# Performance work log

Measured on AMD Instinct MI355X. Metric: run time of the kernel, lower is better.

Reference implementation:

```python
import jax, jax.numpy as jnp
import numpy as np

EPS = 1e-6

def elu_feature_map(x):
    return jax.nn.elu(x) + 1.0

def setup_inputs() -> dict:
    key = jax.random.key(0)
    kq, kk, kv = jax.random.split(key, 3)
    N, L, S, H, D = 8, 8192, 8192, 8, 32
    return {
        "queries": jax.random.normal(kq, (N, L, H, D), dtype=jnp.float32),
        "keys": jax.random.normal(kk, (N, S, H, D), dtype=jnp.float32),
        "values": jax.random.normal(kv, (N, S, H, D), dtype=jnp.float32),
    }

def reference(queries, keys, values):
    # Linear (kernelized) attention, default path of MixAttention.forward
    Q = elu_feature_map(queries)            # [N,L,H,D]
    K = elu_feature_map(keys)               # [N,S,H,D]
    v_length = values.shape[1]
    vals = values / v_length                # [N,S,H,D]
    KV = jnp.einsum('nshd,nshv->nhdv', K, vals)          # [N,H,D,D]
    Z = 1.0 / (jnp.einsum('nlhd,nhd->nlh', Q, K.sum(axis=1)) + EPS)  # [N,L,H]
    out = jnp.einsum('nlhd,nhdv,nlh->nlhv', Q, KV, Z) * v_length     # [N,L,H,D]
    return out
```

## Files before the change

kernel.cpp:

```cpp
#include <hip/hip_runtime.h>


constexpr int N_ = 8, L_ = 8192, S_ = 8192, H_ = 8, D_ = 32;
constexpr int NH = N_ * H_;
constexpr int PART_STRIDE = D_ * D_ + D_;
constexpr int LCH = 256;
constexpr float EPS_ = 1e-6f;
constexpr int HD = H_ * D_;

__device__ __forceinline__ float fmap(float x) {
    return x > 0.0f ? x + 1.0f : __expf(x);
}

template<int SPLIT>
__global__ __launch_bounds__(512, 4) void lin_attn_phase1(
        const float* __restrict__ Kg, const float* __restrict__ Vg,
        float* __restrict__ part) {
    constexpr int CS = S_ / SPLIT;
    const int blk = blockIdx.x;
    const int n  = blk / SPLIT;
    const int sc = blk % SPLIT;
    const int t = threadIdx.x;
    const int w = t >> 6;
    const int j = t & 63;
    const int half = j >> 5;
    const int jj = j & 31;
    const int d0 = (jj & 7) << 2;
    const int v0 = (jj >> 3) << 3;

    float acc[4][8];
    #pragma unroll
    for (int a = 0; a < 4; ++a)
        #pragma unroll
        for (int b = 0; b < 8; ++b) acc[a][b] = 0.0f;
    float kp[4] = {0.f, 0.f, 0.f, 0.f};

    const size_t base = (size_t)n * S_ * HD
                      + (size_t)(sc * CS + half) * HD + w * D_;
    const float* kr = Kg + base + d0;
    const float* vr = Vg + base + v0;
    constexpr int STRIDE = 2 * HD;

#define BEAT(kq, va, vb) do {                                                  \
        float kd[4];                                                           \
        kd[0] = fmap((kq).x); kd[1] = fmap((kq).y);                            \
        kd[2] = fmap((kq).z); kd[3] = fmap((kq).w);                            \
        kp[0] += kd[0]; kp[1] += kd[1]; kp[2] += kd[2]; kp[3] += kd[3];        \
        const float vs[8] = {(va).x, (va).y, (va).z, (va).w,                   \
                             (vb).x, (vb).y, (vb).z, (vb).w};                  \
        _Pragma("unroll")                                                      \
        for (int a = 0; a < 4; ++a)                                            \
            _Pragma("unroll")                                                  \
            for (int bb = 0; bb < 8; ++bb)                                     \
                acc[a][bb] += kd[a] * vs[bb];                                  \
    } while (0)

    float4 kqA = *reinterpret_cast<const float4*>(kr);
    float4 vaA = *reinterpret_cast<const float4*>(vr);
    float4 vbA = *reinterpret_cast<const float4*>(vr + 4);
    float4 kqB = *reinterpret_cast<const float4*>(kr + STRIDE);
    float4 vaB = *reinterpret_cast<const float4*>(vr + STRIDE);
    float4 vbB = *reinterpret_cast<const float4*>(vr + STRIDE + 4);
    kr += 2 * STRIDE; vr += 2 * STRIDE;

    #pragma unroll 1
    for (int b = 0; b < (CS / 2 - 2) / 2; ++b) {
        float4 kqn = *reinterpret_cast<const float4*>(kr);
        float4 van = *reinterpret_cast<const float4*>(vr);
        float4 vbn = *reinterpret_cast<const float4*>(vr + 4);
        BEAT(kqA, vaA, vbA);
        kqA = kqn; vaA = van; vbA = vbn;
        kqn = *reinterpret_cast<const float4*>(kr + STRIDE);
        van = *reinterpret_cast<const float4*>(vr + STRIDE);
        vbn = *reinterpret_cast<const float4*>(vr + STRIDE + 4);
        BEAT(kqB, vaB, vbB);
        kqB = kqn; vaB = van; vbB = vbn;
        kr += 2 * STRIDE; vr += 2 * STRIDE;
    }
    BEAT(kqA, vaA, vbA);
    BEAT(kqB, vaB, vbB);
#undef BEAT

    #pragma unroll
    for (int a = 0; a < 4; ++a)
        #pragma unroll
        for (int bb = 0; bb < 8; ++bb)
            acc[a][bb] += __shfl_xor(acc[a][bb], 32);
    #pragma unroll
    for (int a = 0; a < 4; ++a) kp[a] += __shfl_xor(kp[a], 32);

    if (j < 32) {
        float* P = part + ((size_t)sc * NH + n * H_ + w) * PART_STRIDE;
        #pragma unroll
        for (int a = 0; a < 4; ++a) {
            *reinterpret_cast<float4*>(&P[(d0 + a) * D_ + v0]) =
                make_float4(acc[a][0], acc[a][1], acc[a][2], acc[a][3]);
            *reinterpret_cast<float4*>(&P[(d0 + a) * D_ + v0 + 4]) =
                make_float4(acc[a][4], acc[a][5], acc[a][6], acc[a][7]);
        }
        if (j < 8)
            *reinterpret_cast<float4*>(&P[D_ * D_ + (j << 2)]) =
                make_float4(kp[0], kp[1], kp[2], kp[3]);
    }
}

template<int SPLIT>
__global__ __launch_bounds__(256) void lin_attn_reduce(
        const float* __restrict__ part, float* __restrict__ red) {
    const int i = blockIdx.x * 256 + threadIdx.x;
    if (i >= NH * PART_STRIDE) return;
    float s = 0.0f;
    #pragma unroll 8
    for (int sc = 0; sc < SPLIT; ++sc)
        s += part[(size_t)sc * (NH * PART_STRIDE) + i];
    red[i] = s;
}

__global__ __launch_bounds__(256) void lin_attn_phase2(
        const float* __restrict__ Qg, const float* __restrict__ red,
        float* __restrict__ outg) {
    constexpr int QTS = 32;
    constexpr int NLC = L_ / LCH;
    const int nh  = blockIdx.x / NLC;
    const int lcb = blockIdx.x % NLC;
    const int n = nh / H_, h = nh % H_;
    const int t = threadIdx.x;
    const int v  = t & 31;
    const int rb = t >> 5;
    const int r  = t >> 3;
    const int c  = (t & 7) << 2;

    __shared__ __align__(16) float Qt[QTS][D_];
    __shared__ float zinv_sh[QTS];

    float kv[D_];
    const float* W = red + (size_t)nh * PART_STRIDE;
    #pragma unroll
    for (int d = 0; d < D_; ++d) kv[d] = W[d * D_ + v];
    const float4 ksq = *reinterpret_cast<const float4*>(W + D_ * D_ + c);

    const size_t base = (size_t)n * L_ * H_ * D_ + (size_t)h * D_;
    const int l0 = lcb * LCH;
    for (int step = 0; step < LCH; step += QTS) {
        const float4 q4 = *reinterpret_cast<const float4*>(
            Qg + base + (size_t)(l0 + step + r) * (H_ * D_) + c);
        __syncthreads();
        float4 qf;
        qf.x = fmap(q4.x); qf.y = fmap(q4.y);
        qf.z = fmap(q4.z); qf.w = fmap(q4.w);
        *reinterpret_cast<float4*>(&Qt[r][c]) = qf;
        float zp = qf.x * ksq.x + qf.y * ksq.y + qf.z * ksq.z + qf.w * ksq.w;
        zp += __shfl_xor(zp, 1);
        zp += __shfl_xor(zp, 2);
        zp += __shfl_xor(zp, 4);
        if ((t & 7) == 0) zinv_sh[r] = 1.0f / (zp + EPS_);
        __syncthreads();
        #pragma unroll
        for (int rr = 0; rr < 4; ++rr) {
            const int row = (rr << 3) + rb;
            float acc = 0.0f;
            #pragma unroll
            for (int d2 = 0; d2 < 16; ++d2) {
                const float2 q = *reinterpret_cast<const float2*>(&Qt[row][d2 << 1]);
                acc += q.x * kv[(d2 << 1)] + q.y * kv[(d2 << 1) + 1];
            }
            outg[base + (size_t)(l0 + step + row) * (H_ * D_) + v] =
                acc * zinv_sh[row];
        }
    }
}

extern "C" void kernel_launch(void* const* d_in, const int* in_sizes, int n_in,
                              void* d_out, int out_size, void* d_ws, size_t ws_size,
                              hipStream_t stream) {
    const float* Q = (const float*)d_in[0];
    const float* K = (const float*)d_in[1];
    const float* V = (const float*)d_in[2];
    float* out  = (float*)d_out;
    float* part = (float*)d_ws;

    const size_t need64 = ((size_t)64 + 1) * NH * PART_STRIDE * sizeof(float);
    if (ws_size >= need64) {
        constexpr int SP = 64;
        float* red = part + (size_t)SP * NH * PART_STRIDE;
        lin_attn_phase1<SP><<<N_ * SP, 512, 0, stream>>>(K, V, part);
        lin_attn_reduce<SP><<<(NH * PART_STRIDE + 255) / 256, 256, 0, stream>>>(part, red);
        lin_attn_phase2<<<NH * (L_ / LCH), 256, 0, stream>>>(Q, red, out);
    } else {
        constexpr int SP = 32;
        float* red = part + (size_t)SP * NH * PART_STRIDE;
        lin_attn_phase1<SP><<<N_ * SP, 512, 0, stream>>>(K, V, part);
        lin_attn_reduce<SP><<<(NH * PART_STRIDE + 255) / 256, 256, 0, stream>>>(part, red);
        lin_attn_phase2<<<NH * (L_ / LCH), 256, 0, stream>>>(Q, red, out);
    }
}
```

Before: 88.48 us.

## Stage K/V chunks in LDS via direct global-to-LDS loads in phase1

Phase1 is rewritten so each 256-thread block copies 32-row chunks of K and V into shared memory with global_load_lds DMA. It applies the feature map in place in LDS, then has each 32-thread group compute an 8x4 tile of the KV outer product for one head from shared memory. The cross-half shuffle reduction is gone, and the fallback split drops from 32 to 16. The goal is fewer scattered per-thread global loads and better memory coalescing, but the loop is no longer software-pipelined and adds three barriers per chunk, so load latency is exposed with no double buffering.

```diff
diff --git a/kernel.cpp b/kernel.cpp
--- a/kernel.cpp
+++ b/kernel.cpp
@@ -7,111 +7,101 @@
 constexpr int LCH = 256;
 constexpr float EPS_ = 1e-6f;
 constexpr int HD = H_ * D_;
+constexpr int CHUNK = 32;
 
 __device__ __forceinline__ float fmap(float x) {
     return x > 0.0f ? x + 1.0f : __expf(x);
 }
 
-template<int SPLIT>
-__global__ __launch_bounds__(512, 4) void lin_attn_phase1(
+__device__ __forceinline__ void dma16(const float* g, float* l) {
+    __builtin_amdgcn_global_load_lds(
+        (const __attribute__((address_space(1))) unsigned int*)g,
+        (__attribute__((address_space(3))) unsigned int*)l, 16, 0, 0);
+}
+
+template<int SPL>
+__global__ __launch_bounds__(256, 2) void lin_attn_phase1(
         const float* __restrict__ Kg, const float* __restrict__ Vg,
         float* __restrict__ part) {
-    constexpr int CS = S_ / SPLIT;
+    constexpr int CS_BLK = S_ / SPL;
+    constexpr int ROUNDS = CS_BLK / CHUNK;
     const int blk = blockIdx.x;
-    const int n  = blk / SPLIT;
-    const int sc = blk % SPLIT;
+    const int n = blk / SPL, c = blk % SPL;
     const int t = threadIdx.x;
     const int w = t >> 6;
-    const int j = t & 63;
-    const int half = j >> 5;
-    const int jj = j & 31;
-    const int d0 = (jj & 7) << 2;
-    const int v0 = (jj >> 3) << 3;
+    const int lane = t & 63;
 
-    float acc[4][8];
+    __shared__ __align__(16) float Kt[CHUNK][HD];
+    __shared__ __align__(16) float Vt[CHUNK][HD];
+
+    const int hg = t >> 5;
+    const int i  = t & 31;
+    const int d0 = (i >> 3) << 3;
+    const int v0 = (i & 7) << 2;
+    const int hcol = hg * D_;
+
+    float acc[8][4];
     #pragma unroll
-    for (int a = 0; a < 4; ++a)
+    for (int a = 0; a < 8; ++a)
         #pragma unroll
-        for (int b = 0; b < 8; ++b) acc[a][b] = 0.0f;
-    float kp[4] = {0.f, 0.f, 0.f, 0.f};
+        for (int b = 0; b < 4; ++b) acc[a][b] = 0.0f;
+    float kp = 0.0f;
 
-    const size_t base = (size_t)n * S_ * HD
-                      + (size_t)(sc * CS + half) * HD + w * D_;
-    const float* kr = Kg + base + d0;
-    const float* vr = Vg + base + v0;
-    constexpr int STRIDE = 2 * HD;
+    const float* Kbase = Kg + (size_t)n * S_ * HD + (size_t)c * CS_BLK * HD;
+    const float* Vbase = Vg + (size_t)n * S_ * HD + (size_t)c * CS_BLK * HD;
+    float* Kf = &Kt[0][0];
 
-#define BEAT(kq, va, vb) do {                                                  \
-        float kd[4];                                                           \
-        kd[0] = fmap((kq).x); kd[1] = fmap((kq).y);                            \
-        kd[2] = fmap((kq).z); kd[3] = fmap((kq).w);                            \
-        kp[0] += kd[0]; kp[1] += kd[1]; kp[2] += kd[2]; kp[3] += kd[3];        \
-        const float vs[8] = {(va).x, (va).y, (va).z, (va).w,                   \
-                             (vb).x, (vb).y, (vb).z, (vb).w};                  \
-        _Pragma("unroll")                                                      \
-        for (int a = 0; a < 4; ++a)                                            \
-            _Pragma("unroll")                                                  \
-            for (int bb = 0; bb < 8; ++bb)                                     \
-                acc[a][bb] += kd[a] * vs[bb];                                  \
-    } while (0)
+    for (int r = 0; r < ROUNDS; ++r) {
+        const float* ksrc = Kbase + (size_t)r * CHUNK * HD;
+        const float* vsrc = Vbase + (size_t)r * CHUNK * HD;
+        #pragma unroll
+        for (int q = 0; q < 8; ++q) {
+            const int off = (w * 8 + q) * 256;
+            dma16(ksrc + off + lane * 4, &Kt[0][0] + off);
+            dma16(vsrc + off + lane * 4, &Vt[0][0] + off);
+        }
+        __syncthreads();
 
-    float4 kqA = *reinterpret_cast<const float4*>(kr);
-    float4 vaA = *reinterpret_cast<const float4*>(vr);
-    float4 vbA = *reinterpret_cast<const float4*>(vr + 4);
-    float4 kqB = *reinterpret_cast<const float4*>(kr + STRIDE);
-    float4 vaB = *reinterpret_cast<const float4*>(vr + STRIDE);
-    float4 vbB = *reinterpret_cast<const float4*>(vr + STRIDE + 4);
-    kr += 2 * STRIDE; vr += 2 * STRIDE;
+        #pragma unroll 8
+        for (int k = 0; k < CHUNK; ++k) {
+            const float x = fmap(Kf[t + HD * k]);
+            Kf[t + HD * k] = x;
+            kp += x;
+        }
+        __syncthreads();
 
-    #pragma unroll 1
-    for (int b = 0; b < (CS / 2 - 2) / 2; ++b) {
-        float4 kqn = *reinterpret_cast<const float4*>(kr);
-        float4 van = *reinterpret_cast<const float4*>(vr);
-        float4 vbn = *reinterpret_cast<const float4*>(vr + 4);
-        BEAT(kqA, vaA, vbA);
-        kqA = kqn; vaA = van; vbA = vbn;
-        kqn = *reinterpret_cast<const float4*>(kr + STRIDE);
-        van = *reinterpret_cast<const float4*>(vr + STRIDE);
-        vbn = *reinterpret_cast<const float4*>(vr + STRIDE + 4);
-        BEAT(kqB, vaB, vbB);
-        kqB = kqn; vaB = van; vbB = vbn;
-        kr += 2 * STRIDE; vr += 2 * STRIDE;
+        #pragma unroll 4
+        for (int s = 0; s < CHUNK; ++s) {
+            const float4 ka = *reinterpret_cast<const float4*>(&Kt[s][hcol + d0]);
+            const float4 kb = *reinterpret_cast<const float4*>(&Kt[s][hcol + d0 + 4]);
+            const float4 vq = *reinterpret_cast<const float4*>(&Vt[s][hcol + v0]);
+            const float kd[8] = {ka.x, ka.y, ka.z, ka.w, kb.x, kb.y, kb.z, kb.w};
+            const float vs[4] = {vq.x, vq.y, vq.z, vq.w};
+            #pragma unroll
+            for (int a = 0; a < 8; ++a)
+                #pragma unroll
+                for (int b = 0; b < 4; ++b)
+                    acc[a][b] += kd[a] * vs[b];
+        }
+        __syncthreads();
     }
-    BEAT(kqA, vaA, vbA);
-    BEAT(kqB, vaB, vbB);
-#undef BEAT
 
+    float* P = part + ((size_t)c * NH + n * H_ + hg) * PART_STRIDE;
     #pragma unroll
-    for (int a = 0; a < 4; ++a)
-        #pragma unroll
-        for (int bb = 0; bb < 8; ++bb)
-            acc[a][bb] += __shfl_xor(acc[a][bb], 32);
-    #pragma unroll
-    for (int a = 0; a < 4; ++a) kp[a] += __shfl_xor(kp[a], 32);
-
-    if (j < 32) {
-        float* P = part + ((size_t)sc * NH + n * H_ + w) * PART_STRIDE;
-        #pragma unroll
-        for (int a = 0; a < 4; ++a) {
-            *reinterpret_cast<float4*>(&P[(d0 + a) * D_ + v0]) =
-                make_float4(acc[a][0], acc[a][1], acc[a][2], acc[a][3]);
-            *reinterpret_cast<float4*>(&P[(d0 + a) * D_ + v0 + 4]) =
-                make_float4(acc[a][4], acc[a][5], acc[a][6], acc[a][7]);
-        }
-        if (j < 8)
-            *reinterpret_cast<float4*>(&P[D_ * D_ + (j << 2)]) =
-                make_float4(kp[0], kp[1], kp[2], kp[3]);
-    }
+    for (int a = 0; a < 8; ++a)
+        *reinterpret_cast<float4*>(&P[(d0 + a) * D_ + v0]) =
+            make_float4(acc[a][0], acc[a][1], acc[a][2], acc[a][3]);
+    part[((size_t)c * NH + n * H_ + (t >> 5)) * PART_STRIDE + D_ * D_ + (t & 31)] = kp;
 }
 
-template<int SPLIT>
+template<int SPL>
 __global__ __launch_bounds__(256) void lin_attn_reduce(
         const float* __restrict__ part, float* __restrict__ red) {
     const int i = blockIdx.x * 256 + threadIdx.x;
     if (i >= NH * PART_STRIDE) return;
     float s = 0.0f;
     #pragma unroll 8
-    for (int sc = 0; sc < SPLIT; ++sc)
+    for (int sc = 0; sc < SPL; ++sc)
         s += part[(size_t)sc * (NH * PART_STRIDE) + i];
     red[i] = s;
 }
@@ -183,13 +173,13 @@
     if (ws_size >= need64) {
         constexpr int SP = 64;
         float* red = part + (size_t)SP * NH * PART_STRIDE;
-        lin_attn_phase1<SP><<<N_ * SP, 512, 0, stream>>>(K, V, part);
+        lin_attn_phase1<SP><<<N_ * SP, 256, 0, stream>>>(K, V, part);
         lin_attn_reduce<SP><<<(NH * PART_STRIDE + 255) / 256, 256, 0, stream>>>(part, red);
         lin_attn_phase2<<<NH * (L_ / LCH), 256, 0, stream>>>(Q, red, out);
     } else {
-        constexpr int SP = 32;
+        constexpr int SP = 16;
         float* red = part + (size_t)SP * NH * PART_STRIDE;
-        lin_attn_phase1<SP><<<N_ * SP, 512, 0, stream>>>(K, V, part);
+        lin_attn_phase1<SP><<<N_ * SP, 256, 0, stream>>>(K, V, part);
         lin_attn_reduce<SP><<<(NH * PART_STRIDE + 255) / 256, 256, 0, stream>>>(part, red);
         lin_attn_phase2<<<NH * (L_ / LCH), 256, 0, stream>>>(Q, red, out);
     }
```

Result: faster. 79.77 us (-9.8%).
